# Performance work log

Measured on AMD Instinct MI355X. Metric: run time of the kernel, lower is better.

The kernel has to match this reference:

```python
import jax, jax.numpy as jnp
import numpy as np

N = 100000   # nodes
E = 800000   # edges
H = 4        # heads
C = 32       # out_channels (== in_channels)
IN = 32      # in_channels
ED = 16      # edge_dim
RBF_IN = 42  # sbf_dim*6 (input to lin_rbf)
SBF_IN = 16  # rbf_dim (input to lin_sbf)


def _glorot(key, shape):
    fan_in = shape[0]
    return jax.random.normal(key, shape, dtype=jnp.float32) / np.sqrt(fan_in).astype(np.float32)


def setup_inputs() -> dict:
    key = jax.random.key(0)
    ks = jax.random.split(key, 20)
    inp = {
        "x": jax.random.normal(ks[0], (N, IN), dtype=jnp.float32),
        "edge_attr": jax.random.normal(ks[1], (E, ED), dtype=jnp.float32),
        "rbf": jax.random.normal(ks[2], (N, RBF_IN), dtype=jnp.float32),
        "sbf": jax.random.normal(ks[3], (E, H, SBF_IN), dtype=jnp.float32),
        # params (weights stored [in, out] for y = x @ W)
        "w_rbf0": _glorot(ks[4], (RBF_IN, IN)),
        "w_rbf1": _glorot(ks[5], (IN, IN)),
        "w_sbf0": _glorot(ks[6], (SBF_IN, IN)),
        "w_sbf1": _glorot(ks[7], (IN, IN)),
        "w_ek": _glorot(ks[8], (ED, H * C)),
        "w_ev": _glorot(ks[9], (ED, H * C)),
        "w_k": _glorot(ks[10], (IN, H * C)),
        "b_k": jnp.zeros((H * C,), dtype=jnp.float32),
        "w_q": _glorot(ks[11], (IN, H * C)),
        "b_q": jnp.zeros((H * C,), dtype=jnp.float32),
        "w_v": _glorot(ks[12], (IN, H * C)),
        "b_v": jnp.zeros((H * C,), dtype=jnp.float32),
        "w_skip": _glorot(ks[13], (IN, H * C)),
        "b_skip": jnp.zeros((H * C,), dtype=jnp.float32),
        "edge_index": jax.random.randint(ks[14], (2, E), 0, N, dtype=jnp.int32),
        "edge_index_0": jax.random.randint(ks[15], (E,), 0, N, dtype=jnp.int32),  # unused by forward
    }
    return inp


def reference(x, edge_attr, rbf, sbf,
              w_rbf0, w_rbf1, w_sbf0, w_sbf1,
              w_ek, w_ev, w_k, b_k, w_q, b_q, w_v, b_v,
              w_skip, b_skip, edge_index, edge_index_0):
    src, dst = edge_index[0], edge_index[1]
    # filters (source swaps rbf/sbf naming; we follow forward() exactly)
    rbf_filter = (rbf @ w_rbf0) @ w_rbf1            # [N, IN]
    sbf_filter = (sbf @ w_sbf0) @ w_sbf1            # [E, H, C]

    x_src = rbf_filter * x                          # [N, IN]
    key = (x_src @ w_k + b_k).reshape(-1, H, C)     # [N, H, C]
    query = (x @ w_q + b_q).reshape(-1, H, C)
    value = (x_src @ w_v + b_v).reshape(-1, H, C)

    edge_key = (edge_attr @ w_ek).reshape(-1, H, C)  # [E, H, C]
    edge_val = (edge_attr @ w_ev).reshape(-1, H, C)

    key_j = key[src] + edge_key                     # gather + add [E, H, C]
    value_j = value[src] + edge_val
    query_i = query[dst]

    inv_sqrt_c = np.float32(1.0 / np.sqrt(C))
    alpha = (query_i * key_j).sum(axis=-1) * inv_sqrt_c   # [E, H]

    # segment softmax over destination nodes
    amax = jax.ops.segment_max(alpha, dst, num_segments=N)
    amax = jnp.where(jnp.isfinite(amax), amax, 0.0)
    ex = jnp.exp(alpha - amax[dst])
    denom = jax.ops.segment_sum(ex, dst, num_segments=N)
    alpha = ex / (denom[dst] + np.float32(1e-16))         # [E, H]

    # dropout p=0.0 -> identity
    message = value_j * alpha[:, :, None] * sbf_filter    # [E, H, C]
    aggr = jax.ops.segment_sum(message, dst, num_segments=N)  # [N, H, C]

    out = aggr.reshape(N, H * C) + (x @ w_skip + b_skip)  # concat + root skip
    return out
```

## Files before the change

kernel.cpp:

```cpp
#include <hip/hip_runtime.h>
#include <hip/hip_bf16.h>

#define NN 100000
#define EE 800000
#define SLOT 64

typedef unsigned short u16;

__device__ __forceinline__ float bf2f(u16 u){ return __uint_as_float(((unsigned)u)<<16); }
__device__ __forceinline__ u16 f2bf(float f){
  unsigned u = __float_as_uint(f);
  u += 0x7fffu + ((u>>16)&1u);
  return (u16)(u>>16);
}
__device__ __forceinline__ float lo16(unsigned v){ return __uint_as_float(v<<16); }
__device__ __forceinline__ float hi16(unsigned v){ return __uint_as_float(v & 0xffff0000u); }

__device__ __forceinline__ void cvt8(uint4 u, float* f){
  f[0]=lo16(u.x); f[1]=hi16(u.x);
  f[2]=lo16(u.y); f[3]=hi16(u.y);
  f[4]=lo16(u.z); f[5]=hi16(u.z);
  f[6]=lo16(u.w); f[7]=hi16(u.w);
}

__device__ __forceinline__ float rdlanef(float v, int k){
  return __uint_as_float(__builtin_amdgcn_readlane(__float_as_uint(v), k));
}

__global__ void kprep(const float* w_rbf0, const float* w_rbf1, const float* w_sbf0, const float* w_sbf1,
                      const float* w_k, const float* b_k, const float* w_q, const float* b_q,
                      const float* w_v, const float* b_v, const float* w_skip, const float* b_skip,
                      float* Wrbfc, float* Wsbfc,
                      float2* wkv, float2* wqs, float2* bkv, float2* bqs)
{
  int b = blockIdx.x;
  if (b==0){
    for (int idx=threadIdx.x; idx<42*32; idx+=blockDim.x){
      int k=idx>>5, c=idx&31;
      float acc=0.f;
      for (int j=0;j<32;j++) acc += w_rbf0[k*32+j]*w_rbf1[j*32+c];
      Wrbfc[idx]=acc;
    }
  } else if (b==1){
    for (int idx=threadIdx.x; idx<16*32; idx+=blockDim.x){
      int k=idx>>5, c=idx&31;
      float acc=0.f;
      for (int j=0;j<32;j++) acc += w_sbf0[k*32+j]*w_sbf1[j*32+c];
      Wsbfc[idx]=acc;
    }
  } else if (b==2){
    for (int idx=threadIdx.x; idx<4096; idx+=blockDim.x){
      wkv[idx]=make_float2(w_k[idx], w_v[idx]);
      wqs[idx]=make_float2(w_q[idx], w_skip[idx]);
    }
  } else {
    for (int idx=threadIdx.x; idx<128; idx+=blockDim.x){
      bkv[idx]=make_float2(b_k[idx], b_v[idx]);
      bqs[idx]=make_float2(b_q[idx], b_skip[idx]);
    }
  }
}

__global__ void kscatter(const int* ei, int* cnt, int* slots){
  int e = blockIdx.x*blockDim.x + threadIdx.x;
  if (e < EE){
    int dst = ei[EE+e];
    int pos = atomicAdd(&cnt[dst], 1);
    if (pos < SLOT) slots[(long)dst*SLOT+pos] = e;
  }
}

__global__ void __launch_bounds__(256) knode(const float* x, const float* rbf, const float* Wrbfc,
                                             const float2* wkv_g, const float2* wqs_g,
                                             const float2* bkv_g, const float2* bqs_g,
                                             u16* key, u16* value, u16* query, float* outp)
{
  __shared__ float2 wkv[4096];
  __shared__ float2 wqs[4096];
  __shared__ float  Wr[42*32];
  __shared__ float2 bkv[128], bqs[128];
  __shared__ float  xs[2][32], xsrcs[2][32], rbfs[2][42];
  for (int i=threadIdx.x;i<4096;i+=256){ wkv[i]=wkv_g[i]; wqs[i]=wqs_g[i]; }
  for (int i=threadIdx.x;i<1344;i+=256) Wr[i]=Wrbfc[i];
  if (threadIdx.x<128){ bkv[threadIdx.x]=bkv_g[threadIdx.x]; bqs[threadIdx.x]=bqs_g[threadIdx.x]; }
  __syncthreads();
  int half = threadIdx.x>>7, t = threadIdx.x&127;
  for (long p = blockIdx.x; p*2 < NN; p += gridDim.x){
    long n = p*2 + half;
    if (t<32)                xs[half][t]      = x[n*32+t];
    else if (t>=64 && t<106) rbfs[half][t-64] = rbf[n*42+(t-64)];
    __syncthreads();
    if (t<32){
      float acc=0.f;
      #pragma unroll
      for (int k=0;k<42;k++) acc += rbfs[half][k]*Wr[k*32+t];
      xsrcs[half][t] = acc*xs[half][t];
    }
    __syncthreads();
    {
      float2 b1 = bkv[t], b2 = bqs[t];
      float ak=b1.x, av=b1.y, aq=b2.x, as=b2.y;
      #pragma unroll
      for (int k=0;k<32;k++){
        float xv = xsrcs[half][k];
        float xq = xs[half][k];
        float2 w1 = wkv[(k<<7)+t];
        float2 w2 = wqs[(k<<7)+t];
        ak += xv*w1.x; av += xv*w1.y;
        aq += xq*w2.x; as += xq*w2.y;
      }
      key  [n*128+t] = f2bf(ak);
      value[n*128+t] = f2bf(av);
      query[n*128+t] = f2bf(aq);
      outp [n*128+t] = as;
    }
    __syncthreads();
  }
}

__global__ void __launch_bounds__(256) kalpha2(const float* edge_attr, const int* ei,
                                               const float* wek_g, const u16* key, const u16* query,
                                               float* alpha)
{
  __shared__ __align__(16) float wek[2048];
  __shared__ float eas[64][17];
  __shared__ int srcs[64], dsts[64];
  for (int idx=threadIdx.x; idx<2048; idx+=256) wek[idx]=wek_g[idx];
  int g = threadIdx.x>>4, l = threadIdx.x&15;
  int h = l>>2;
  for (long base=(long)blockIdx.x*64; base<EE; base+=(long)gridDim.x*64){
    __syncthreads();
    {
      const float4* s4 = (const float4*)(edge_attr + base*16);
      float4 v = s4[threadIdx.x];
      int e = threadIdx.x>>2, c0 = (threadIdx.x&3)<<2;
      eas[e][c0]=v.x; eas[e][c0+1]=v.y; eas[e][c0+2]=v.z; eas[e][c0+3]=v.w;
      if (threadIdx.x < 64)       srcs[threadIdx.x]    = ei[base + threadIdx.x];
      else if (threadIdx.x < 128) dsts[threadIdx.x-64] = ei[EE + base + threadIdx.x-64];
    }
    __syncthreads();
    float ek[4][8];
    #pragma unroll
    for (int j=0;j<4;j++){
      #pragma unroll
      for (int i=0;i<8;i++) ek[j][i]=0.f;
    }
    #pragma unroll
    for (int k=0;k<16;k++){
      const float4* w4 = (const float4*)&wek[(k<<7)+(l<<3)];
      float4 wa=w4[0], wb=w4[1];
      #pragma unroll
      for (int j=0;j<4;j++){
        float ea = eas[(g<<2)+j][k];
        ek[j][0]+=ea*wa.x; ek[j][1]+=ea*wa.y; ek[j][2]+=ea*wa.z; ek[j][3]+=ea*wa.w;
        ek[j][4]+=ea*wb.x; ek[j][5]+=ea*wb.y; ek[j][6]+=ea*wb.z; ek[j][7]+=ea*wb.w;
      }
    }
    #pragma unroll
    for (int j=0;j<4;j++){
      int el = (g<<2)+j;
      long e = base + el;
      int src = srcs[el], dst = dsts[el];
      float q8[8], k8[8];
      uint4 ku = *(const uint4*)(key   + (long)src*128 + l*8);
      uint4 qu = *(const uint4*)(query + (long)dst*128 + l*8);
      cvt8(ku,k8); cvt8(qu,q8);
      float part=0.f;
      #pragma unroll
      for (int i=0;i<8;i++) part += q8[i]*(k8[i]+ek[j][i]);
      part += __shfl_xor(part,1);
      part += __shfl_xor(part,2);
      if ((l&3)==0) alpha[e*4+h] = part*0.17677669529663687f;
    }
  }
}

__global__ void __launch_bounds__(256,4) kaggr_wave(const float* edge_attr, const float* sbf,
                                                    const int* ei, const float* wev_g, const float* Wsbfc,
                                                    const u16* value, const float* alpha,
                                                    const int* cnt, const int* slots, float* outp)
{
  __shared__ float4 wlds[4][SLOT];
  __shared__ float  sstage[4][64];
  int wid = threadIdx.x>>6;
  int l   = threadIdx.x&63;
  int dst = blockIdx.x*4 + wid;
  int c = cnt[dst]; if (c > SLOT) c = SLOT;
  if (c == 0) return;
  int h = l>>4;

  float2 wv[16], ws[16];
  #pragma unroll
  for (int k=0;k<16;k++){
    wv[k] = *(const float2*)&wev_g[k*128 + 2*l];
    ws[k] = *(const float2*)&Wsbfc[k*32 + ((2*l)&31)];
  }

  const int* sl = slots + (long)dst*SLOT;
  int e_l = 0, src_l = 0;
  if (l < c){ e_l = sl[l]; src_l = ei[e_l]; }

  float4 araw = make_float4(-3.0e38f,-3.0e38f,-3.0e38f,-3.0e38f);
  if (l < c) araw = *(const float4*)(alpha + (long)e_l*4);

  int eN = __builtin_amdgcn_readlane(e_l, 0);
  int sN = __builtin_amdgcn_readlane(src_l, 0);
  float    earN = edge_attr[(long)eN*16 + (l&15)];
  float    svN  = sbf[(long)eN*64 + l];
  unsigned vvN  = *(const unsigned*)(value + (long)sN*128 + 2*l);

  float4 m4 = araw;
  #pragma unroll
  for (int off=1; off<=32; off<<=1){
    m4.x = fmaxf(m4.x, __shfl_xor(m4.x, off));
    m4.y = fmaxf(m4.y, __shfl_xor(m4.y, off));
    m4.z = fmaxf(m4.z, __shfl_xor(m4.z, off));
    m4.w = fmaxf(m4.w, __shfl_xor(m4.w, off));
  }
  float4 ex4 = make_float4(0.f,0.f,0.f,0.f);
  if (l < c){
    ex4.x = __expf(araw.x - m4.x);
    ex4.y = __expf(araw.y - m4.y);
    ex4.z = __expf(araw.z - m4.z);
    ex4.w = __expf(araw.w - m4.w);
  }
  float4 d4 = ex4;
  #pragma unroll
  for (int off=1; off<=32; off<<=1){
    d4.x += __shfl_xor(d4.x, off);
    d4.y += __shfl_xor(d4.y, off);
    d4.z += __shfl_xor(d4.z, off);
    d4.w += __shfl_xor(d4.w, off);
  }
  if (l < c){
    float4 w4;
    w4.x = ex4.x / (d4.x + 1e-16f);
    w4.y = ex4.y / (d4.y + 1e-16f);
    w4.z = ex4.z / (d4.z + 1e-16f);
    w4.w = ex4.w / (d4.w + 1e-16f);
    wlds[wid][l] = w4;
  }

  float2 seed = *(const float2*)(outp + (long)dst*128 + 2*l);
  float acc0 = seed.x, acc1 = seed.y;

  for (int i=0;i<c;i++){
    float ear = earN; float sv = svN; unsigned vv = vvN;
    sstage[wid][l] = sv;
    if (i+1 < c){
      int e1 = __builtin_amdgcn_readlane(e_l, i+1);
      int s1 = __builtin_amdgcn_readlane(src_l, i+1);
      earN = edge_attr[(long)e1*16 + (l&15)];
      svN  = sbf[(long)e1*64 + l];
      vvN  = *(const unsigned*)(value + (long)s1*128 + 2*l);
    }
    float w = *((const float*)&wlds[wid][i] + h);
    const float4* sp = (const float4*)&sstage[wid][h<<4];
    float4 sq0 = sp[0], sq1 = sp[1], sq2 = sp[2], sq3 = sp[3];
    float sarr[16] = {sq0.x,sq0.y,sq0.z,sq0.w, sq1.x,sq1.y,sq1.z,sq1.w,
                      sq2.x,sq2.y,sq2.z,sq2.w, sq3.x,sq3.y,sq3.z,sq3.w};
    float ev0=0.f, ev1=0.f, f0=0.f, f1=0.f;
    #pragma unroll
    for (int k=0;k<16;k++){
      float eak = rdlanef(ear, k);
      ev0 += eak*wv[k].x; ev1 += eak*wv[k].y;
      f0  += sarr[k]*ws[k].x; f1 += sarr[k]*ws[k].y;
    }
    float v0 = lo16(vv), v1 = hi16(vv);
    acc0 += (v0+ev0)*(w*f0);
    acc1 += (v1+ev1)*(w*f1);
  }

  *(float2*)(outp + (long)dst*128 + 2*l) = make_float2(acc0, acc1);
}

extern "C" void kernel_launch(void* const* d_in, const int* in_sizes, int n_in,
                              void* d_out, int out_size, void* d_ws, size_t ws_size,
                              hipStream_t stream)
{
  const float* x         = (const float*)d_in[0];
  const float* edge_attr = (const float*)d_in[1];
  const float* rbf       = (const float*)d_in[2];
  const float* sbf       = (const float*)d_in[3];
  const float* w_rbf0    = (const float*)d_in[4];
  const float* w_rbf1    = (const float*)d_in[5];
  const float* w_sbf0    = (const float*)d_in[6];
  const float* w_sbf1    = (const float*)d_in[7];
  const float* w_ek      = (const float*)d_in[8];
  const float* w_ev      = (const float*)d_in[9];
  const float* w_k       = (const float*)d_in[10];
  const float* b_k       = (const float*)d_in[11];
  const float* w_q       = (const float*)d_in[12];
  const float* b_q       = (const float*)d_in[13];
  const float* w_v       = (const float*)d_in[14];
  const float* b_v       = (const float*)d_in[15];
  const float* w_skip    = (const float*)d_in[16];
  const float* b_skip    = (const float*)d_in[17];
  const int* ei          = (const int*)d_in[18];
  float* out = (float*)d_out;

  char* ws = (char*)d_ws;
  u16*   key   = (u16*)  (ws + 0);
  u16*   query = (u16*)  (ws + 25600000);
  u16*   value = (u16*)  (ws + 51200000);
  float* alpha = (float*)(ws + 76800000);
  int*   slots = (int*)  (ws + 89600000);
  int*   cnt   = (int*)  (ws + 115200000);
  float* Wrbfc = (float*)(ws + 115600000);
  float* Wsbfc = (float*)(ws + 115608192);
  float2* wkv  = (float2*)(ws + 115612288);
  float2* wqs  = (float2*)(ws + 115645056);
  float2* bkv  = (float2*)(ws + 115677824);
  float2* bqs  = (float2*)(ws + 115678848);

  kprep<<<4,256,0,stream>>>(w_rbf0,w_rbf1,w_sbf0,w_sbf1,w_k,b_k,w_q,b_q,w_v,b_v,w_skip,b_skip,
                            Wrbfc,Wsbfc,wkv,wqs,bkv,bqs);
  hipMemsetAsync(cnt, 0, NN*sizeof(int), stream);
  kscatter<<<3125,256,0,stream>>>(ei, cnt, slots);
  knode<<<1024,256,0,stream>>>(x,rbf,Wrbfc,wkv,wqs,bkv,bqs,key,value,query,out);
  kalpha2<<<2500,256,0,stream>>>(edge_attr,ei,w_ek,key,query,alpha);
  kaggr_wave<<<25000,256,0,stream>>>(edge_attr,sbf,ei,w_ev,Wsbfc,value,alpha,cnt,slots,out);
}
```

Baseline: 980.4 us.

## Split node projection into xsrc pass and register-tiled GEMM, persistent aggregation waves

The rbf filter times x product moves into its own kernel, writing a buffer that a new node-projection kernel reads. In that kernel each wave handles four nodes and broadcasts inputs with readlane, so every weight read from shared memory is reused four times and the per-node block barriers are gone. The aggregation kernel becomes a grid-stride persistent loop over 2048 blocks, so the sbf-filter and edge-value weight registers are loaded once per wave rather than once per destination. The cost is an extra kernel launch, an extra global round trip for the xsrc buffer, and higher register pressure in the node kernel.

```diff
diff --git a/kernel.cpp b/kernel.cpp
--- a/kernel.cpp
+++ b/kernel.cpp
@@ -70,51 +70,66 @@
   }
 }
 
-__global__ void __launch_bounds__(256) knode(const float* x, const float* rbf, const float* Wrbfc,
-                                             const float2* wkv_g, const float2* wqs_g,
-                                             const float2* bkv_g, const float2* bqs_g,
-                                             u16* key, u16* value, u16* query, float* outp)
+__global__ void __launch_bounds__(256) kxsrc(const float* x, const float* rbf, const float* Wrbfc,
+                                             float* xsrcb)
+{
+  __shared__ float Wr[1344];
+  for (int i=threadIdx.x;i<1344;i+=256) Wr[i]=Wrbfc[i];
+  __syncthreads();
+  int n = blockIdx.x*8 + (threadIdx.x>>5), c = threadIdx.x&31;
+  const float* rrow = rbf + (long)n*42;
+  float acc=0.f;
+  #pragma unroll
+  for (int k=0;k<42;k++) acc += rrow[k]*Wr[k*32+c];
+  xsrcb[(long)n*32+c] = acc * x[(long)n*32+c];
+}
+
+__global__ void __launch_bounds__(256) knode2(const float* x, const float* xsrcb,
+                                              const float2* wkv_g, const float2* wqs_g,
+                                              const float2* bkv_g, const float2* bqs_g,
+                                              u16* key, u16* value, u16* query, float* outp)
 {
   __shared__ float2 wkv[4096];
   __shared__ float2 wqs[4096];
-  __shared__ float  Wr[42*32];
-  __shared__ float2 bkv[128], bqs[128];
-  __shared__ float  xs[2][32], xsrcs[2][32], rbfs[2][42];
   for (int i=threadIdx.x;i<4096;i+=256){ wkv[i]=wkv_g[i]; wqs[i]=wqs_g[i]; }
-  for (int i=threadIdx.x;i<1344;i+=256) Wr[i]=Wrbfc[i];
-  if (threadIdx.x<128){ bkv[threadIdx.x]=bkv_g[threadIdx.x]; bqs[threadIdx.x]=bqs_g[threadIdx.x]; }
   __syncthreads();
-  int half = threadIdx.x>>7, t = threadIdx.x&127;
-  for (long p = blockIdx.x; p*2 < NN; p += gridDim.x){
-    long n = p*2 + half;
-    if (t<32)                xs[half][t]      = x[n*32+t];
-    else if (t>=64 && t<106) rbfs[half][t-64] = rbf[n*42+(t-64)];
-    __syncthreads();
-    if (t<32){
-      float acc=0.f;
-      #pragma unroll
-      for (int k=0;k<42;k++) acc += rbfs[half][k]*Wr[k*32+t];
-      xsrcs[half][t] = acc*xs[half][t];
-    }
-    __syncthreads();
-    {
-      float2 b1 = bkv[t], b2 = bqs[t];
-      float ak=b1.x, av=b1.y, aq=b2.x, as=b2.y;
-      #pragma unroll
-      for (int k=0;k<32;k++){
-        float xv = xsrcs[half][k];
-        float xq = xs[half][k];
-        float2 w1 = wkv[(k<<7)+t];
-        float2 w2 = wqs[(k<<7)+t];
-        ak += xv*w1.x; av += xv*w1.y;
-        aq += xq*w2.x; as += xq*w2.y;
+  int wid = threadIdx.x>>6, l = threadIdx.x&63;
+  float2 bkl = bkv_g[l], bkh = bkv_g[64+l];
+  float2 bql = bqs_g[l], bqh = bqs_g[64+l];
+  int nw = gridDim.x*4;
+  for (int g = blockIdx.x*4+wid; g < NN/4; g += nw){
+    long b = (long)g*128;
+    float xqa = x[b+l],      xqb = x[b+64+l];
+    float xva = xsrcb[b+l],  xvb = xsrcb[b+64+l];
+    float2 aK[4][2], aQ[4][2];
+    #pragma unroll
+    for (int j=0;j<4;j++){ aK[j][0]=bkl; aK[j][1]=bkh; aQ[j][0]=bql; aQ[j][1]=bqh; }
+    #pragma unroll
+    for (int k=0;k<32;k++){
+      float2 w1l = wkv[(k<<7)+l], w1h = wkv[(k<<7)+64+l];
+      float2 w2l = wqs[(k<<7)+l], w2h = wqs[(k<<7)+64+l];
+      #pragma unroll
+      for (int j=0;j<4;j++){
+        float xv = (j<2) ? rdlanef(xva, j*32+k) : rdlanef(xvb, (j-2)*32+k);
+        float xq = (j<2) ? rdlanef(xqa, j*32+k) : rdlanef(xqb, (j-2)*32+k);
+        aK[j][0].x += xv*w1l.x; aK[j][0].y += xv*w1l.y;
+        aK[j][1].x += xv*w1h.x; aK[j][1].y += xv*w1h.y;
+        aQ[j][0].x += xq*w2l.x; aQ[j][0].y += xq*w2l.y;
+        aQ[j][1].x += xq*w2h.x; aQ[j][1].y += xq*w2h.y;
       }
-      key  [n*128+t] = f2bf(ak);
-      value[n*128+t] = f2bf(av);
-      query[n*128+t] = f2bf(aq);
-      outp [n*128+t] = as;
-    }
-    __syncthreads();
+    }
+    #pragma unroll
+    for (int j=0;j<4;j++){
+      long n = (long)g*4 + j;
+      key  [n*128+l]    = f2bf(aK[j][0].x);
+      key  [n*128+64+l] = f2bf(aK[j][1].x);
+      value[n*128+l]    = f2bf(aK[j][0].y);
+      value[n*128+64+l] = f2bf(aK[j][1].y);
+      query[n*128+l]    = f2bf(aQ[j][0].x);
+      query[n*128+64+l] = f2bf(aQ[j][1].x);
+      outp [n*128+l]    = aQ[j][0].y;
+      outp [n*128+64+l] = aQ[j][1].y;
+    }
   }
 }
 
@@ -184,9 +199,6 @@
   __shared__ float  sstage[4][64];
   int wid = threadIdx.x>>6;
   int l   = threadIdx.x&63;
-  int dst = blockIdx.x*4 + wid;
-  int c = cnt[dst]; if (c > SLOT) c = SLOT;
-  if (c == 0) return;
   int h = l>>4;
 
   float2 wv[16], ws[16];
@@ -196,82 +208,88 @@
     ws[k] = *(const float2*)&Wsbfc[k*32 + ((2*l)&31)];
   }
 
-  const int* sl = slots + (long)dst*SLOT;
-  int e_l = 0, src_l = 0;
-  if (l < c){ e_l = sl[l]; src_l = ei[e_l]; }
-
-  float4 araw = make_float4(-3.0e38f,-3.0e38f,-3.0e38f,-3.0e38f);
-  if (l < c) araw = *(const float4*)(alpha + (long)e_l*4);
-
-  int eN = __builtin_amdgcn_readlane(e_l, 0);
-  int sN = __builtin_amdgcn_readlane(src_l, 0);
-  float    earN = edge_attr[(long)eN*16 + (l&15)];
-  float    svN  = sbf[(long)eN*64 + l];
-  unsigned vvN  = *(const unsigned*)(value + (long)sN*128 + 2*l);
-
-  float4 m4 = araw;
-  #pragma unroll
-  for (int off=1; off<=32; off<<=1){
-    m4.x = fmaxf(m4.x, __shfl_xor(m4.x, off));
-    m4.y = fmaxf(m4.y, __shfl_xor(m4.y, off));
-    m4.z = fmaxf(m4.z, __shfl_xor(m4.z, off));
-    m4.w = fmaxf(m4.w, __shfl_xor(m4.w, off));
-  }
-  float4 ex4 = make_float4(0.f,0.f,0.f,0.f);
-  if (l < c){
-    ex4.x = __expf(araw.x - m4.x);
-    ex4.y = __expf(araw.y - m4.y);
-    ex4.z = __expf(araw.z - m4.z);
-    ex4.w = __expf(araw.w - m4.w);
-  }
-  float4 d4 = ex4;
-  #pragma unroll
-  for (int off=1; off<=32; off<<=1){
-    d4.x += __shfl_xor(d4.x, off);
-    d4.y += __shfl_xor(d4.y, off);
-    d4.z += __shfl_xor(d4.z, off);
-    d4.w += __shfl_xor(d4.w, off);
-  }
-  if (l < c){
-    float4 w4;
-    w4.x = ex4.x / (d4.x + 1e-16f);
-    w4.y = ex4.y / (d4.y + 1e-16f);
-    w4.z = ex4.z / (d4.z + 1e-16f);
-    w4.w = ex4.w / (d4.w + 1e-16f);
-    wlds[wid][l] = w4;
-  }
-
-  float2 seed = *(const float2*)(outp + (long)dst*128 + 2*l);
-  float acc0 = seed.x, acc1 = seed.y;
-
-  for (int i=0;i<c;i++){
-    float ear = earN; float sv = svN; unsigned vv = vvN;
-    sstage[wid][l] = sv;
-    if (i+1 < c){
-      int e1 = __builtin_amdgcn_readlane(e_l, i+1);
-      int s1 = __builtin_amdgcn_readlane(src_l, i+1);
-      earN = edge_attr[(long)e1*16 + (l&15)];
-      svN  = sbf[(long)e1*64 + l];
-      vvN  = *(const unsigned*)(value + (long)s1*128 + 2*l);
-    }
-    float w = *((const float*)&wlds[wid][i] + h);
-    const float4* sp = (const float4*)&sstage[wid][h<<4];
-    float4 sq0 = sp[0], sq1 = sp[1], sq2 = sp[2], sq3 = sp[3];
-    float sarr[16] = {sq0.x,sq0.y,sq0.z,sq0.w, sq1.x,sq1.y,sq1.z,sq1.w,
-                      sq2.x,sq2.y,sq2.z,sq2.w, sq3.x,sq3.y,sq3.z,sq3.w};
-    float ev0=0.f, ev1=0.f, f0=0.f, f1=0.f;
-    #pragma unroll
-    for (int k=0;k<16;k++){
-      float eak = rdlanef(ear, k);
-      ev0 += eak*wv[k].x; ev1 += eak*wv[k].y;
-      f0  += sarr[k]*ws[k].x; f1 += sarr[k]*ws[k].y;
-    }
-    float v0 = lo16(vv), v1 = hi16(vv);
-    acc0 += (v0+ev0)*(w*f0);
-    acc1 += (v1+ev1)*(w*f1);
-  }
-
-  *(float2*)(outp + (long)dst*128 + 2*l) = make_float2(acc0, acc1);
+  int nwaves = gridDim.x*4;
+  for (int dst = blockIdx.x*4 + wid; dst < NN; dst += nwaves){
+    int c = cnt[dst]; if (c > SLOT) c = SLOT;
+    if (c == 0) continue;
+
+    const int* sl = slots + (long)dst*SLOT;
+    int e_l = 0, src_l = 0;
+    if (l < c){ e_l = sl[l]; src_l = ei[e_l]; }
+
+    float4 araw = make_float4(-3.0e38f,-3.0e38f,-3.0e38f,-3.0e38f);
+    if (l < c) araw = *(const float4*)(alpha + (long)e_l*4);
+
+    int eN = __builtin_amdgcn_readlane(e_l, 0);
+    int sN = __builtin_amdgcn_readlane(src_l, 0);
+    float    earN = edge_attr[(long)eN*16 + (l&15)];
+    float    svN  = sbf[(long)eN*64 + l];
+    unsigned vvN  = *(const unsigned*)(value + (long)sN*128 + 2*l);
+
+    float4 m4 = araw;
+    #pragma unroll
+    for (int off=1; off<=32; off<<=1){
+      m4.x = fmaxf(m4.x, __shfl_xor(m4.x, off));
+      m4.y = fmaxf(m4.y, __shfl_xor(m4.y, off));
+      m4.z = fmaxf(m4.z, __shfl_xor(m4.z, off));
+      m4.w = fmaxf(m4.w, __shfl_xor(m4.w, off));
+    }
+    float4 ex4 = make_float4(0.f,0.f,0.f,0.f);
+    if (l < c){
+      ex4.x = __expf(araw.x - m4.x);
+      ex4.y = __expf(araw.y - m4.y);
+      ex4.z = __expf(araw.z - m4.z);
+      ex4.w = __expf(araw.w - m4.w);
+    }
+    float4 d4 = ex4;
+    #pragma unroll
+    for (int off=1; off<=32; off<<=1){
+      d4.x += __shfl_xor(d4.x, off);
+      d4.y += __shfl_xor(d4.y, off);
+      d4.z += __shfl_xor(d4.z, off);
+      d4.w += __shfl_xor(d4.w, off);
+    }
+    if (l < c){
+      float4 w4;
+      w4.x = ex4.x / (d4.x + 1e-16f);
+      w4.y = ex4.y / (d4.y + 1e-16f);
+      w4.z = ex4.z / (d4.z + 1e-16f);
+      w4.w = ex4.w / (d4.w + 1e-16f);
+      wlds[wid][l] = w4;
+    }
+
+    float2 seed = *(const float2*)(outp + (long)dst*128 + 2*l);
+    float acc0 = seed.x, acc1 = seed.y;
+
+    for (int i=0;i<c;i++){
+      float ear = earN; float sv = svN; unsigned vv = vvN;
+      sstage[wid][l] = sv;
+      if (i+1 < c){
+        int e1 = __builtin_amdgcn_readlane(e_l, i+1);
+        int s1 = __builtin_amdgcn_readlane(src_l, i+1);
+        earN = edge_attr[(long)e1*16 + (l&15)];
+        svN  = sbf[(long)e1*64 + l];
+        vvN  = *(const unsigned*)(value + (long)s1*128 + 2*l);
+      }
+      float w = *((const float*)&wlds[wid][i] + h);
+      const float4* sp = (const float4*)&sstage[wid][h<<4];
+      float4 sq0 = sp[0], sq1 = sp[1], sq2 = sp[2], sq3 = sp[3];
+      float sarr[16] = {sq0.x,sq0.y,sq0.z,sq0.w, sq1.x,sq1.y,sq1.z,sq1.w,
+                        sq2.x,sq2.y,sq2.z,sq2.w, sq3.x,sq3.y,sq3.z,sq3.w};
+      float ev0=0.f, ev1=0.f, f0=0.f, f1=0.f;
+      #pragma unroll
+      for (int k=0;k<16;k++){
+        float eak = rdlanef(ear, k);
+        ev0 += eak*wv[k].x; ev1 += eak*wv[k].y;
+        f0  += sarr[k]*ws[k].x; f1 += sarr[k]*ws[k].y;
+      }
+      float v0 = lo16(vv), v1 = hi16(vv);
+      acc0 += (v0+ev0)*(w*f0);
+      acc1 += (v1+ev1)*(w*f1);
+    }
+
+    *(float2*)(outp + (long)dst*128 + 2*l) = make_float2(acc0, acc1);
+  }
 }
 
 extern "C" void kernel_launch(void* const* d_in, const int* in_sizes, int n_in,
@@ -312,12 +330,14 @@
   float2* wqs  = (float2*)(ws + 115645056);
   float2* bkv  = (float2*)(ws + 115677824);
   float2* bqs  = (float2*)(ws + 115678848);
+  float* xsrcb = (float*)(ws + 115680256);
 
   kprep<<<4,256,0,stream>>>(w_rbf0,w_rbf1,w_sbf0,w_sbf1,w_k,b_k,w_q,b_q,w_v,b_v,w_skip,b_skip,
                             Wrbfc,Wsbfc,wkv,wqs,bkv,bqs);
   hipMemsetAsync(cnt, 0, NN*sizeof(int), stream);
   kscatter<<<3125,256,0,stream>>>(ei, cnt, slots);
-  knode<<<1024,256,0,stream>>>(x,rbf,Wrbfc,wkv,wqs,bkv,bqs,key,value,query,out);
+  kxsrc<<<12500,256,0,stream>>>(x, rbf, Wrbfc, xsrcb);
+  knode2<<<512,256,0,stream>>>(x, xsrcb, wkv, wqs, bkv, bqs, key, value, query, out);
   kalpha2<<<2500,256,0,stream>>>(edge_attr,ei,w_ek,key,query,alpha);
-  kaggr_wave<<<25000,256,0,stream>>>(edge_attr,sbf,ei,w_ev,Wsbfc,value,alpha,cnt,slots,out);
-}
+  kaggr_wave<<<2048,256,0,stream>>>(edge_attr,sbf,ei,w_ev,Wsbfc,value,alpha,cnt,slots,out);
+}
```

New measurement: 878.0 us. -10.4%, faster.
